# Optimization experiments

Hardware: AMD Instinct MI355X
Metric: run time of the kernel (lower is better)

## Reference

```python
import jax, jax.numpy as jnp
import numpy as np

B, T, C, H = 4, 2048, 1024, 16
D = C // H  # head_dim = 64


def setup_inputs() -> dict:
    key = jax.random.key(0)
    k1, k2, k3, k4, k5 = jax.random.split(key, 5)
    x = jax.random.normal(k1, (B, T, C), dtype=jnp.float32)
    # torch nn.Linear weights: [out_features, in_features]
    s = 1.0 / np.sqrt(C)
    qkv_w = jax.random.uniform(k2, (3 * C, C), dtype=jnp.float32, minval=-s, maxval=s)
    qkv_b = jax.random.uniform(k3, (3 * C,), dtype=jnp.float32, minval=-s, maxval=s)
    out_w = jax.random.uniform(k4, (C, C), dtype=jnp.float32, minval=-s, maxval=s)
    out_b = jax.random.uniform(k5, (C,), dtype=jnp.float32, minval=-s, maxval=s)
    # causal mask broadcastable to [B,H,T,T]; 0 (False) marks masked positions
    attn_mask = jnp.tril(jnp.ones((T, T), dtype=bool))[None, None]
    return {"x": x, "qkv_w": qkv_w, "qkv_b": qkv_b, "out_w": out_w,
            "out_b": out_b, "attn_mask": attn_mask}


def reference(x, qkv_w, qkv_b, out_w, out_b, attn_mask):
    qkv = x @ qkv_w.T + qkv_b                      # [B,T,3C]
    q, k, v = jnp.split(qkv, 3, axis=-1)
    # [B,T,C] -> [B,H,T,D]
    q = q.reshape(B, T, H, D).transpose(0, 2, 1, 3)
    k = k.reshape(B, T, H, D).transpose(0, 2, 1, 3)
    v = v.reshape(B, T, H, D).transpose(0, 2, 1, 3)
    scale = 1.0 / np.sqrt(D)
    attn = jnp.einsum('bhqd,bhkd->bhqk', q, k) * scale   # [B,H,T,T]
    neg = jnp.finfo(attn.dtype).min
    attn = jnp.where(attn_mask, attn, neg)
    attn = jax.nn.softmax(attn, axis=-1)
    out = jnp.einsum('bhqk,bhkd->bhqd', attn, v)          # [B,H,T,D]
    out = out.transpose(0, 2, 1, 3).reshape(B, T, C)
    return out @ out_w.T + out_b
```

## Files before the change

kernel.cpp:

```cpp
#include <hip/hip_runtime.h>
#include <hip/hip_bf16.h>

#define B_ 4
#define T_ 2048
#define C_ 1024
#define H_ 16
#define D_ 64

typedef __hip_bfloat16 bf16;
typedef float f32x4 __attribute__((ext_vector_type(4)));
typedef short bf16s8 __attribute__((ext_vector_type(8)));

#define NEG_BIG (-1e30f)

__device__ inline unsigned short f2bf(float f) {
  __hip_bfloat16 h = __float2bfloat16(f);
  return *reinterpret_cast<unsigned short*>(&h);
}
__device__ inline float bf_lo(unsigned u) {
  union { unsigned u; float f; } c; c.u = u << 16; return c.f;
}

__device__ inline void async_load16(const void* g, void* l) {
  __builtin_amdgcn_global_load_lds(
      (const __attribute__((address_space(1))) unsigned int*)g,
      (__attribute__((address_space(3))) unsigned int*)l, 16, 0, 0);
}

__device__ inline void plswap32(unsigned& a, unsigned& b) {
  auto r = __builtin_amdgcn_permlane32_swap(a, b, false, false);
  a = r[0]; b = r[1];
}
__device__ inline void plswap16(unsigned& a, unsigned& b) {
  auto r = __builtin_amdgcn_permlane16_swap(a, b, false, false);
  a = r[0]; b = r[1];
}

union U4 { uint4 u; unsigned short s[8]; };

__device__ inline uint4 load8(const void* base, size_t idx, int f32) {
  if (f32) {
    const float* p = (const float*)base + idx;
    float4 a = *(const float4*)p;
    float4 b = *(const float4*)(p + 4);
    U4 r;
    r.s[0] = f2bf(a.x); r.s[1] = f2bf(a.y); r.s[2] = f2bf(a.z); r.s[3] = f2bf(a.w);
    r.s[4] = f2bf(b.x); r.s[5] = f2bf(b.y); r.s[6] = f2bf(b.z); r.s[7] = f2bf(b.w);
    return r.u;
  }
  return *(const uint4*)((const unsigned short*)base + idx);
}

__global__ void detect_k(const unsigned short* __restrict__ w, int* __restrict__ flag) {
  int lane = threadIdx.x;
  bool big = false;
  for (int i = lane; i < 512; i += 64) {
    float f = bf_lo((unsigned)w[i]);
    if (!(fabsf(f) <= 1.0f)) big = true;
  }
  int any = __any(big);
  if (lane == 0) *flag = any ? 1 : 0;
}

#define R_X   1048576
#define R_WQ  (R_X + 393216)
#define R_WO  (R_WQ + 131072)
#define R_BQ  (R_WO + 384)
#define R_BO  (R_BQ + 128)
__global__ __launch_bounds__(256) void convert_all_k(
    const void* __restrict__ x, const void* __restrict__ wq,
    const void* __restrict__ wo, const void* __restrict__ bq,
    const void* __restrict__ bo,
    bf16* __restrict__ xd, bf16* __restrict__ wqd, bf16* __restrict__ wod,
    bf16* __restrict__ bqd, bf16* __restrict__ bod,
    const int* __restrict__ flag) {
  const int f32 = *flag;
  long long g = (long long)blockIdx.x * 256 + threadIdx.x;
  if (g >= R_BO) return;
  const void* src; bf16* dst; long long base;
  if (g < R_X)       { src = x;  dst = xd;  base = 0; }
  else if (g < R_WQ) { src = wq; dst = wqd; base = R_X; }
  else if (g < R_WO) { src = wo; dst = wod; base = R_WQ; }
  else if (g < R_BQ) { src = bq; dst = bqd; base = R_WO; }
  else               { src = bo; dst = bod; base = R_BQ; }
  size_t i = (size_t)(g - base) * 8;
  *(uint4*)(dst + i) = load8(src, i, f32);
}

template <int KDIM, int MROWS>
__device__ inline void gemm_core(const bf16* __restrict__ A,
                                 const bf16* __restrict__ W,
                                 int tm, int tn, int wm, int wn,
                                 f32x4 acc[MROWS / 32][4], bf16* As, bf16* Bs) {
  const int tid  = threadIdx.x;
  const int lane = tid & 63;
  const int rl   = lane & 15;
  const int kq   = (lane >> 4) * 8;

  for (int k0 = 0; k0 < KDIM; k0 += 32) {
    __syncthreads();
#pragma unroll
    for (int j = 0; j < MROWS / 64; ++j) {
      int f    = j * 4096 + tid * 16;
      int row  = f >> 6;
      int colb = f & 63;
      async_load16((const char*)A + ((size_t)(tm + row) * KDIM + k0) * 2 + colb,
                   (char*)As + f);
    }
#pragma unroll
    for (int j = 0; j < 2; ++j) {
      int f    = j * 4096 + tid * 16;
      int row  = f >> 6;
      int colb = f & 63;
      async_load16((const char*)W + ((size_t)(tn + row) * KDIM + k0) * 2 + colb,
                   (char*)Bs + f);
    }
    __syncthreads();

    bf16s8 af[MROWS / 32], bw[4];
#pragma unroll
    for (int mt = 0; mt < MROWS / 32; ++mt)
      af[mt] = *(const bf16s8*)(As + (wm + mt * 16 + rl) * 32 + kq);
#pragma unroll
    for (int nt = 0; nt < 4; ++nt)
      bw[nt] = *(const bf16s8*)(Bs + (wn + nt * 16 + rl) * 32 + kq);

#pragma unroll
    for (int mt = 0; mt < MROWS / 32; ++mt)
#pragma unroll
      for (int nt = 0; nt < 4; ++nt)
        acc[mt][nt] = __builtin_amdgcn_mfma_f32_16x16x32_bf16(af[mt], bw[nt],
                                                              acc[mt][nt], 0, 0, 0);
  }
}

#define CSTRIDE 72
#define FSTRIDE 68

__global__ __launch_bounds__(256) void gemm_qkv_k(
    const bf16* __restrict__ X, const bf16* __restrict__ W,
    const bf16* __restrict__ bias,
    bf16* __restrict__ q, bf16* __restrict__ k, bf16* __restrict__ v) {
  __shared__ __align__(16) char smem[4 * 64 * CSTRIDE * 2];
  bf16* As = (bf16*)smem;
  bf16* Bs = (bf16*)(smem + 8192);
  const int tid = threadIdx.x;
  const int wave = tid >> 6, lane = tid & 63;
  const int tm = blockIdx.x * 128, tn = blockIdx.y * 128;
  const int wm = (wave >> 1) * 64, wn = (wave & 1) * 64;
  f32x4 acc[4][4];
#pragma unroll
  for (int i = 0; i < 4; ++i)
#pragma unroll
    for (int j = 0; j < 4; ++j) acc[i][j] = 0.0f;

  gemm_core<C_, 128>(X, W, tm, tn, wm, wn, acc, As, Bs);

  __syncthreads();
  bf16* Cs = (bf16*)smem + wave * 64 * CSTRIDE;

  const int rl = lane & 15, qd = lane >> 4;
  const int nbase = tn + wn;
  const int which = nbase >> 10;
  const int h = (nbase & 1023) >> 6;
  const float sc = which == 0 ? 0.125f : 1.0f;
  const int mbase = tm + wm;
  const int b = mbase >> 11, t0 = mbase & 2047;
  bf16* dst = which == 0 ? q : (which == 1 ? k : v);
  bf16* base = dst + (((size_t)(b * H_ + h)) * T_ + t0) * D_;

#pragma unroll
  for (int nt = 0; nt < 4; ++nt) {
    float bv = __bfloat162float(bias[nbase + nt * 16 + rl]);
#pragma unroll
    for (int mt = 0; mt < 4; ++mt)
#pragma unroll
      for (int r = 0; r < 4; ++r)
        Cs[(mt * 16 + qd * 4 + r) * CSTRIDE + nt * 16 + rl] =
            __float2bfloat16((acc[mt][nt][r] + bv) * sc);
  }
#pragma unroll
  for (int it = 0; it < 8; ++it) {
    int row = it * 8 + (lane >> 3);
    uint4 val = *(const uint4*)(Cs + row * CSTRIDE + (lane & 7) * 8);
    *(uint4*)(base + row * D_ + (lane & 7) * 8) = val;
  }
}

__global__ __launch_bounds__(256) void gemm_out_k(
    const bf16* __restrict__ O, const bf16* __restrict__ W,
    const bf16* __restrict__ bias, const int* __restrict__ flag,
    void* __restrict__ out) {
  __shared__ __align__(16) char smem[4 * 32 * FSTRIDE * 4];
  bf16* As = (bf16*)smem;
  bf16* Bs = (bf16*)(smem + 4096);
  const int f32 = *flag;
  const int tid = threadIdx.x;
  const int wave = tid >> 6, lane = tid & 63;
  const int tm = blockIdx.x * 64, tn = blockIdx.y * 128;
  const int wm = (wave >> 1) * 32, wn = (wave & 1) * 64;
  f32x4 acc[2][4];
#pragma unroll
  for (int i = 0; i < 2; ++i)
#pragma unroll
    for (int j = 0; j < 4; ++j) acc[i][j] = 0.0f;

  gemm_core<C_, 64>(O, W, tm, tn, wm, wn, acc, As, Bs);

  __syncthreads();
  const int rl = lane & 15, qd = lane >> 4;

  if (f32) {
    float* Cs = (float*)(smem + wave * 32 * FSTRIDE * 4);
#pragma unroll
    for (int nt = 0; nt < 4; ++nt) {
      float bv = __bfloat162float(bias[tn + wn + nt * 16 + rl]);
#pragma unroll
      for (int mt = 0; mt < 2; ++mt)
#pragma unroll
        for (int r = 0; r < 4; ++r)
          Cs[(mt * 16 + qd * 4 + r) * FSTRIDE + nt * 16 + rl] = acc[mt][nt][r] + bv;
    }
    float* obase = (float*)out + (size_t)(tm + wm) * C_ + tn + wn;
#pragma unroll
    for (int it = 0; it < 8; ++it) {
      int row = it * 4 + (lane >> 4);
      float4 val = *(const float4*)(Cs + row * FSTRIDE + (lane & 15) * 4);
      *(float4*)(obase + (size_t)row * C_ + (lane & 15) * 4) = val;
    }
  } else {
    bf16* Cs = (bf16*)(smem + wave * 32 * FSTRIDE * 4);
#pragma unroll
    for (int nt = 0; nt < 4; ++nt) {
      float bv = __bfloat162float(bias[tn + wn + nt * 16 + rl]);
#pragma unroll
      for (int mt = 0; mt < 2; ++mt)
#pragma unroll
        for (int r = 0; r < 4; ++r)
          Cs[(mt * 16 + qd * 4 + r) * CSTRIDE + nt * 16 + rl] =
              __float2bfloat16(acc[mt][nt][r] + bv);
    }
    bf16* obase = (bf16*)out + (size_t)(tm + wm) * C_ + tn + wn;
#pragma unroll
    for (int it = 0; it < 4; ++it) {
      int row = it * 8 + (lane >> 3);
      uint4 val = *(const uint4*)(Cs + row * CSTRIDE + (lane & 7) * 8);
      *(uint4*)(obase + (size_t)row * C_ + (lane & 7) * 8) = val;
    }
  }
}

__global__ __launch_bounds__(256) void fattn_k(
    const bf16* __restrict__ q, const bf16* __restrict__ k,
    const bf16* __restrict__ v, bf16* __restrict__ o) {
  __shared__ __align__(16) bf16 Ks[64 * 64];
  __shared__ __align__(16) bf16 Vs[64 * 64];
  const int tid = threadIdx.x, wave = tid >> 6, lane = tid & 63;
  const int rl = lane & 15, quad = lane >> 4;
  const int bh = blockIdx.x;
  const int b = bh >> 4, h = bh & 15;
  const size_t bhT = (size_t)bh * T_;
  const int sw0 = (quad ^ (rl & 7)) << 3;
  const int sw1 = ((quad | 4) ^ (rl & 7)) << 3;

  bf16s8 ones;
#pragma unroll
  for (int i = 0; i < 8; ++i) ones[i] = (short)0x3F80;

  const int qb = 31 - blockIdx.y;
  const int q0 = qb * 64;

  const int kr0 = tid >> 3;
  const int kc0 = ((tid & 7) ^ (kr0 & 7)) << 4;
  const char* kstage = (const char*)k + (bhT + kr0) * (D_ * 2) + kc0;
  char* kdst = (char*)Ks + tid * 16;

  const bf16* qr = q + (bhT + q0 + wave * 16 + rl) * D_;
  bf16s8 qf0 = *(const bf16s8*)(qr + quad * 8);
  bf16s8 qf1 = *(const bf16s8*)(qr + 32 + quad * 8);

  f32x4 oacc[4], lacc;
#pragma unroll
  for (int nt = 0; nt < 4; ++nt) oacc[nt] = 0.0f;
  lacc = 0.0f;

  const int nchunk = qb + 1;
#pragma unroll 1
  for (int c = 0; c < nchunk; ++c) {
    const int k0 = c << 6;
    __syncthreads();
    async_load16(kstage + (size_t)k0 * 128, kdst);
    async_load16(kstage + (size_t)(k0 + 32) * 128, kdst + 4096);
    {
      int kp = tid & 31;
      int dg = tid >> 5;
      uint4 va = *(const uint4*)(v + (bhT + k0 + 2 * kp) * D_ + dg * 8);
      uint4 vb = *(const uint4*)(v + (bhT + k0 + 2 * kp + 1) * D_ + dg * 8);
      const unsigned* au = (const unsigned*)&va;
      const unsigned* bu = (const unsigned*)&vb;
#pragma unroll
      for (int m = 0; m < 4; ++m) {
        unsigned lo = (au[m] & 0xffffu) | (bu[m] << 16);
        unsigned hi = (au[m] >> 16) | (bu[m] & 0xffff0000u);
        int d0 = dg * 8 + 2 * m;
        int o0 = d0 * 64 + (((kp >> 2) ^ (2 * m)) << 3) + 2 * (kp & 3);
        int o1 = (d0 + 1) * 64 + (((kp >> 2) ^ (2 * m + 1)) << 3) + 2 * (kp & 3);
        *(unsigned*)(Vs + o0) = lo;
        *(unsigned*)(Vs + o1) = hi;
      }
    }
    __syncthreads();

    const int t0 = q0 + wave * 16;

    f32x4 s[4];
#pragma unroll
    for (int nt = 0; nt < 4; ++nt) s[nt] = 0.0f;
#pragma unroll
    for (int nt = 0; nt < 4; ++nt) {
      int key = nt * 16 + rl;
      bf16s8 kb0 = *(const bf16s8*)(Ks + key * 64 + sw0);
      bf16s8 kb1 = *(const bf16s8*)(Ks + key * 64 + sw1);
      s[nt] = __builtin_amdgcn_mfma_f32_16x16x32_bf16(kb0, qf0, s[nt], 0, 0, 0);
      s[nt] = __builtin_amdgcn_mfma_f32_16x16x32_bf16(kb1, qf1, s[nt], 0, 0, 0);
    }

    if (c == nchunk - 1) {
      int t = t0 + rl;
#pragma unroll
      for (int nt = 0; nt < 4; ++nt)
#pragma unroll
        for (int r = 0; r < 4; ++r) {
          int key = k0 + nt * 16 + quad * 4 + r;
          if (key > t) s[nt][r] = NEG_BIG;
        }
    }

    unsigned pk[4][2];
#pragma unroll
    for (int nt = 0; nt < 4; ++nt) {
#pragma unroll
      for (int r = 0; r < 4; ++r)
        s[nt][r] = __expf(fminf(s[nt][r], 30.0f));
      pk[nt][0] = (unsigned)f2bf(s[nt][0]) | ((unsigned)f2bf(s[nt][1]) << 16);
      pk[nt][1] = (unsigned)f2bf(s[nt][2]) | ((unsigned)f2bf(s[nt][3]) << 16);
    }

    union { unsigned w[4]; bf16s8 v; } u0, u1;
    {
      unsigned a = pk[0][0], bq_ = pk[1][0];
      plswap32(a, bq_); plswap16(a, bq_);
      u0.w[0] = a; u0.w[2] = bq_;
      a = pk[0][1]; bq_ = pk[1][1];
      plswap32(a, bq_); plswap16(a, bq_);
      u0.w[1] = a; u0.w[3] = bq_;
      a = pk[2][0]; bq_ = pk[3][0];
      plswap32(a, bq_); plswap16(a, bq_);
      u1.w[0] = a; u1.w[2] = bq_;
      a = pk[2][1]; bq_ = pk[3][1];
      plswap32(a, bq_); plswap16(a, bq_);
      u1.w[1] = a; u1.w[3] = bq_;
    }
    bf16s8 pa0 = u0.v, pa1 = u1.v;

    lacc = __builtin_amdgcn_mfma_f32_16x16x32_bf16(pa0, ones, lacc, 0, 0, 0);
    lacc = __builtin_amdgcn_mfma_f32_16x16x32_bf16(pa1, ones, lacc, 0, 0, 0);
#pragma unroll
    for (int nt = 0; nt < 4; ++nt) {
      int d = nt * 16 + rl;
      bf16s8 vb0 = *(const bf16s8*)(Vs + d * 64 + sw0);
      bf16s8 vb1 = *(const bf16s8*)(Vs + d * 64 + sw1);
      oacc[nt] = __builtin_amdgcn_mfma_f32_16x16x32_bf16(pa0, vb0, oacc[nt], 0, 0, 0);
      oacc[nt] = __builtin_amdgcn_mfma_f32_16x16x32_bf16(pa1, vb1, oacc[nt], 0, 0, 0);
    }
  }

  f32x4 linv;
#pragma unroll
  for (int r = 0; r < 4; ++r) linv[r] = 1.0f / lacc[r];
#pragma unroll
  for (int nt = 0; nt < 4; ++nt) {
    int d = nt * 16 + rl;
#pragma unroll
    for (int r = 0; r < 4; ++r) {
      int t = q0 + wave * 16 + quad * 4 + r;
      o[((size_t)b * T_ + t) * C_ + h * D_ + d] =
          __float2bfloat16(oacc[nt][r] * linv[r]);
    }
  }
}

extern "C" void kernel_launch(void* const* d_in, const int* in_sizes, int n_in,
                              void* d_out, int out_size, void* d_ws, size_t ws_size,
                              hipStream_t stream) {
  (void)in_sizes; (void)n_in; (void)out_size; (void)ws_size;
  const void* x     = d_in[0];
  const void* qkv_w = d_in[1];
  const void* qkv_b = d_in[2];
  const void* out_w = d_in[3];
  const void* out_b = d_in[4];

  const size_t nqkv = (size_t)B_ * T_ * C_;
  char* ws = (char*)d_ws;
  int*  flag = (int*)ws;
  bf16* q   = (bf16*)(ws + 256);
  bf16* kk  = q + nqkv;
  bf16* vv  = kk + nqkv;
  bf16* oo  = vv + nqkv;
  bf16* xbf = oo;
  bf16* wqkv = oo + nqkv;
  bf16* wout = wqkv + 3 * C_ * C_;
  bf16* bqkv = wout + C_ * C_;
  bf16* bout = bqkv + 3 * C_;

  detect_k<<<1, 64, 0, stream>>>((const unsigned short*)qkv_w, flag);
  convert_all_k<<<(R_BO + 255) / 256, 256, 0, stream>>>(
      x, qkv_w, out_w, qkv_b, out_b, xbf, wqkv, wout, bqkv, bout, flag);

  gemm_qkv_k<<<dim3(64, 24), 256, 0, stream>>>(xbf, wqkv, bqkv, q, kk, vv);
  fattn_k<<<dim3(64, 32), 256, 0, stream>>>(q, kk, vv, oo);
  gemm_out_k<<<dim3(128, 8), 256, 0, stream>>>(oo, wout, bout, flag, d_out);
}
```

Baseline: 273.2 us.

## Double-buffer K/V tiles in flash attention to overlap loads with compute

Splits the K and V shared-memory tiles into two buffers. The next chunk's K (via async global-to-LDS loads) and V (into registers) is fetched before the current chunk's MFMA work, and V is written into the alternate buffer after compute. This cuts the per-iteration syncs from two to one and aims to hide global load latency behind QK/PV math. In exchange it doubles LDS use (32KB per block), which may lower occupancy, and holds the prefetched V in extra registers.

```diff
diff --git a/kernel.cpp b/kernel.cpp
--- a/kernel.cpp
+++ b/kernel.cpp
@@ -253,8 +253,8 @@
 __global__ __launch_bounds__(256) void fattn_k(
     const bf16* __restrict__ q, const bf16* __restrict__ k,
     const bf16* __restrict__ v, bf16* __restrict__ o) {
-  __shared__ __align__(16) bf16 Ks[64 * 64];
-  __shared__ __align__(16) bf16 Vs[64 * 64];
+  __shared__ __align__(16) bf16 Ks[2][64 * 64];
+  __shared__ __align__(16) bf16 Vs[2][64 * 64];
   const int tid = threadIdx.x, wave = tid >> 6, lane = tid & 63;
   const int rl = lane & 15, quad = lane >> 4;
   const int bh = blockIdx.x;
@@ -273,7 +273,9 @@
   const int kr0 = tid >> 3;
   const int kc0 = ((tid & 7) ^ (kr0 & 7)) << 4;
   const char* kstage = (const char*)k + (bhT + kr0) * (D_ * 2) + kc0;
-  char* kdst = (char*)Ks + tid * 16;
+
+  const int kp = tid & 31, dg = tid >> 5;
+  const bf16* vstage = v + (bhT + 2 * kp) * D_ + dg * 8;
 
   const bf16* qr = q + (bhT + q0 + wave * 16 + rl) * D_;
   bf16s8 qf0 = *(const bf16s8*)(qr + quad * 8);
@@ -285,33 +287,47 @@
   lacc = 0.0f;
 
   const int nchunk = qb + 1;
+
+  {
+    async_load16(kstage, (char*)Ks[0] + tid * 16);
+    async_load16(kstage + 32 * 128, (char*)Ks[0] + 4096 + tid * 16);
+    uint4 va = *(const uint4*)(vstage);
+    uint4 vb = *(const uint4*)(vstage + D_);
+    const unsigned* au = (const unsigned*)&va;
+    const unsigned* bu = (const unsigned*)&vb;
+#pragma unroll
+    for (int m = 0; m < 4; ++m) {
+      unsigned lo = (au[m] & 0xffffu) | (bu[m] << 16);
+      unsigned hi = (au[m] >> 16) | (bu[m] & 0xffff0000u);
+      int d0 = dg * 8 + 2 * m;
+      int o0 = d0 * 64 + (((kp >> 2) ^ (2 * m)) << 3) + 2 * (kp & 3);
+      int o1 = (d0 + 1) * 64 + (((kp >> 2) ^ (2 * m + 1)) << 3) + 2 * (kp & 3);
+      *(unsigned*)(Vs[0] + o0) = lo;
+      *(unsigned*)(Vs[0] + o1) = hi;
+    }
+  }
+  __syncthreads();
+
+  int cur = 0;
 #pragma unroll 1
   for (int c = 0; c < nchunk; ++c) {
+    const bf16* Kc = Ks[cur];
+    const bf16* Vc = Vs[cur];
+    const bool pf = (c + 1 < nchunk);
+
+    uint4 va, vb;
+    if (pf) {
+      const char* ks = kstage + (size_t)(c + 1) * 8192;
+      char* kd = (char*)Ks[cur ^ 1] + tid * 16;
+      async_load16(ks, kd);
+      async_load16(ks + 32 * 128, kd + 4096);
+      const bf16* vs = vstage + (size_t)(c + 1) * 4096;
+      va = *(const uint4*)(vs);
+      vb = *(const uint4*)(vs + D_);
+    }
+
+    const int t0 = q0 + wave * 16;
     const int k0 = c << 6;
-    __syncthreads();
-    async_load16(kstage + (size_t)k0 * 128, kdst);
-    async_load16(kstage + (size_t)(k0 + 32) * 128, kdst + 4096);
-    {
-      int kp = tid & 31;
-      int dg = tid >> 5;
-      uint4 va = *(const uint4*)(v + (bhT + k0 + 2 * kp) * D_ + dg * 8);
-      uint4 vb = *(const uint4*)(v + (bhT + k0 + 2 * kp + 1) * D_ + dg * 8);
-      const unsigned* au = (const unsigned*)&va;
-      const unsigned* bu = (const unsigned*)&vb;
-#pragma unroll
-      for (int m = 0; m < 4; ++m) {
-        unsigned lo = (au[m] & 0xffffu) | (bu[m] << 16);
-        unsigned hi = (au[m] >> 16) | (bu[m] & 0xffff0000u);
-        int d0 = dg * 8 + 2 * m;
-        int o0 = d0 * 64 + (((kp >> 2) ^ (2 * m)) << 3) + 2 * (kp & 3);
-        int o1 = (d0 + 1) * 64 + (((kp >> 2) ^ (2 * m + 1)) << 3) + 2 * (kp & 3);
-        *(unsigned*)(Vs + o0) = lo;
-        *(unsigned*)(Vs + o1) = hi;
-      }
-    }
-    __syncthreads();
-
-    const int t0 = q0 + wave * 16;
 
     f32x4 s[4];
 #pragma unroll
@@ -319,8 +335,8 @@
 #pragma unroll
     for (int nt = 0; nt < 4; ++nt) {
       int key = nt * 16 + rl;
-      bf16s8 kb0 = *(const bf16s8*)(Ks + key * 64 + sw0);
-      bf16s8 kb1 = *(const bf16s8*)(Ks + key * 64 + sw1);
+      bf16s8 kb0 = *(const bf16s8*)(Kc + key * 64 + sw0);
+      bf16s8 kb1 = *(const bf16s8*)(Kc + key * 64 + sw1);
       s[nt] = __builtin_amdgcn_mfma_f32_16x16x32_bf16(kb0, qf0, s[nt], 0, 0, 0);
       s[nt] = __builtin_amdgcn_mfma_f32_16x16x32_bf16(kb1, qf1, s[nt], 0, 0, 0);
     }
@@ -368,11 +384,29 @@
 #pragma unroll
     for (int nt = 0; nt < 4; ++nt) {
       int d = nt * 16 + rl;
-      bf16s8 vb0 = *(const bf16s8*)(Vs + d * 64 + sw0);
-      bf16s8 vb1 = *(const bf16s8*)(Vs + d * 64 + sw1);
+      bf16s8 vb0 = *(const bf16s8*)(Vc + d * 64 + sw0);
+      bf16s8 vb1 = *(const bf16s8*)(Vc + d * 64 + sw1);
       oacc[nt] = __builtin_amdgcn_mfma_f32_16x16x32_bf16(pa0, vb0, oacc[nt], 0, 0, 0);
       oacc[nt] = __builtin_amdgcn_mfma_f32_16x16x32_bf16(pa1, vb1, oacc[nt], 0, 0, 0);
     }
+
+    if (pf) {
+      bf16* Vn = Vs[cur ^ 1];
+      const unsigned* au = (const unsigned*)&va;
+      const unsigned* bu = (const unsigned*)&vb;
+#pragma unroll
+      for (int m = 0; m < 4; ++m) {
+        unsigned lo = (au[m] & 0xffffu) | (bu[m] << 16);
+        unsigned hi = (au[m] >> 16) | (bu[m] & 0xffff0000u);
+        int d0 = dg * 8 + 2 * m;
+        int o0 = d0 * 64 + (((kp >> 2) ^ (2 * m)) << 3) + 2 * (kp & 3);
+        int o1 = (d0 + 1) * 64 + (((kp >> 2) ^ (2 * m + 1)) << 3) + 2 * (kp & 3);
+        *(unsigned*)(Vn + o0) = lo;
+        *(unsigned*)(Vn + o1) = hi;
+      }
+    }
+    __syncthreads();
+    cur ^= 1;
   }
 
   f32x4 linv;
```

New measurement: 271.7 us. About the same (-0.6%).
